# Kernel optimization log

Hardware: AMD Instinct MI355X
Metric: run time of the kernel (lower is better)

## Reference

```python
import jax, jax.numpy as jnp
import numpy as np

HARMONICS = 5


def _harmonic_basis(x):
    k = jnp.arange(1, HARMONICS + 1, dtype=x.dtype)            # [H]
    kx = x[..., None] * k                                       # [B, D, H]
    sc = jnp.stack([jnp.sin(kx), jnp.cos(kx)], axis=-1)         # [B, D, H, 2]
    sc = sc.reshape(*x.shape, 2 * HARMONICS)                    # interleaved sin/cos
    ones = jnp.ones((*x.shape, 1), dtype=x.dtype)
    return jnp.concatenate([ones, sc], axis=-1)                 # [B, D, 2H+1]


def setup_inputs() -> dict:
    key = jax.random.key(0)
    k1, k2, k3 = jax.random.split(key, 3)
    B, D, F, H = 16384, 256, 11, 256
    x = jax.random.normal(k1, (B, D), dtype=jnp.float32)
    W = jax.random.normal(k2, (D, F, H), dtype=jnp.float32) * (1.0 / np.sqrt(F))
    b = jax.random.normal(k3, (D, H), dtype=jnp.float32) * 0.01
    return {"x": x, "W": W, "b": b}


def reference(x, W, b) -> jnp.ndarray:
    # basis expansion per feature, batched small GEMM, summed over features
    basis = _harmonic_basis(x)                                  # [B, D, F]
    out = jnp.einsum('bdf,dfh->bh', basis, W)                   # sum over features fused
    out = out + jnp.sum(b, axis=0)                              # sum of per-feature biases
    return out
```

## Files before the change

kernel.cpp:

```cpp
#include <hip/hip_runtime.h>
#include <hip/hip_bf16.h>


#define BDIM 16384
#define DDIM 256
#define HOUT 256
#define KTOT 2560
#define NKT  80
#define BM 64
#define BN 128

typedef __bf16 bf16x8 __attribute__((ext_vector_type(8)));
typedef float floatx4 __attribute__((ext_vector_type(4)));

__device__ __forceinline__ unsigned short f2bf(float f) {
    unsigned int u = __float_as_uint(f);
    return (unsigned short)((u + 0x7FFFu + ((u >> 16) & 1u)) >> 16);
}

__device__ __forceinline__ unsigned int pkbf(float a, float b) {
    __hip_bfloat162 r = __float22bfloat162_rn(make_float2(a, b));
    return *reinterpret_cast<unsigned int*>(&r);
}

__global__ void prep_kernel(const float* __restrict__ W, const float* __restrict__ bias,
                            unsigned short* __restrict__ Wfrag, float* __restrict__ c_part) {
    const int bid = blockIdx.x;
    const int t = threadIdx.x;
    if (bid < NKT) {
        const int kt = bid;
        const int dtile = kt / 10;
        const int f = kt - dtile * 10 + 1;
        const float* wsrc = W + ((size_t)(dtile * 32) * 11 + f) * 256 + t;
        union { unsigned short s[32]; int4 v[4]; } buf;
#pragma unroll
        for (int dd = 0; dd < 32; ++dd)
            buf.s[dd] = f2bf(wsrc[(size_t)dd * 11 * 256]);
        int4* dst = (int4*)(Wfrag + ((size_t)kt * 256 + t) * 32);
#pragma unroll
        for (int v = 0; v < 4; ++v) dst[v] = buf.v[v];
    } else {
        const int p = bid - NKT;
        float acc = 0.f;
#pragma unroll
        for (int dd = 0; dd < 32; ++dd) {
            const int d = p * 32 + dd;
            acc += W[(size_t)(d * 11) * 256 + t] + bias[(size_t)d * 256 + t];
        }
        c_part[p * 256 + t] = acc;
    }
}

__global__ __launch_bounds__(256, 2)
void kan_gemm(const float* __restrict__ x, const unsigned short* __restrict__ Wfrag,
              const float* __restrict__ c_part, float* __restrict__ out) {
    __shared__ unsigned short As[10 * 4 * 512];

    const int t = threadIdx.x;
    const int m0 = blockIdx.x * BM;
    const int h0 = blockIdx.y * BN;

    const int lane = t & 63;
    const int wave = t >> 6;
    const int wr = wave >> 1;
    const int wc = wave & 1;
    const int l15 = lane & 15;
    const int koff = lane >> 4;

    const int m_a = lane;
    const int q = wave;
    const int it_w = m_a >> 4;
    const int slot = (m_a & 15) + 16 * q;

    floatx4 acc[2][4];
#pragma unroll
    for (int i = 0; i < 2; ++i)
#pragma unroll
        for (int j = 0; j < 4; ++j)
            acc[i][j] = (floatx4){0.f, 0.f, 0.f, 0.f};

    const float* xrow = x + (size_t)(m0 + m_a) * DDIM;
    const unsigned short* bbase = Wfrag + (size_t)(h0 + wc * 64 + l15) * 32 + koff * 8;

    float4 xa = *(const float4*)(xrow + q * 8);
    float4 xb = *(const float4*)(xrow + q * 8 + 4);

    for (int dtile = 0; dtile < 8; ++dtile) {
        float xv[8] = {xa.x, xa.y, xa.z, xa.w, xb.x, xb.y, xb.z, xb.w};
        float sc[8], cc[8], sp[8], cp[8], t2c[8];
#pragma unroll
        for (int j = 0; j < 8; ++j) {
            __sincosf(xv[j], &sc[j], &cc[j]);
            t2c[j] = cc[j] + cc[j];
            sp[j] = 0.f;
            cp[j] = 1.f;
        }
#pragma unroll
        for (int k = 1; k <= 5; ++k) {
            union { unsigned int u[4]; int4 v; } vs, vc;
#pragma unroll
            for (int p = 0; p < 4; ++p) {
                vs.u[p] = pkbf(sc[2 * p], sc[2 * p + 1]);
                vc.u[p] = pkbf(cc[2 * p], cc[2 * p + 1]);
            }
            *(int4*)(&As[((2 * k - 2) * 4 + it_w) * 512 + slot * 8]) = vs.v;
            *(int4*)(&As[((2 * k - 1) * 4 + it_w) * 512 + slot * 8]) = vc.v;
            if (k < 5) {
#pragma unroll
                for (int j = 0; j < 8; ++j) {
                    const float ns = t2c[j] * sc[j] - sp[j];
                    const float nc = t2c[j] * cc[j] - cp[j];
                    sp[j] = sc[j]; cp[j] = cc[j];
                    sc[j] = ns;   cc[j] = nc;
                }
            }
        }
        __syncthreads();

        if (dtile < 7) {
            xa = *(const float4*)(xrow + (dtile + 1) * 32 + q * 8);
            xb = *(const float4*)(xrow + (dtile + 1) * 32 + q * 8 + 4);
        }

        const unsigned short* bkt = bbase + (size_t)(dtile * 10) * 8192;

        bf16x8 bf0[4], bf1[4], af0[2], af1[2];
#pragma unroll
        for (int j = 0; j < 4; ++j)
            bf0[j] = *(const bf16x8*)(bkt + j * 512);
#pragma unroll
        for (int i = 0; i < 2; ++i)
            af0[i] = *(const bf16x8*)(&As[(0 * 4 + wr * 2 + i) * 512 + lane * 8]);

#pragma unroll
        for (int hs = 0; hs < 10; ++hs) {
            bf16x8* bnext = (hs & 1) ? bf0 : bf1;
            bf16x8* anext = (hs & 1) ? af0 : af1;
            if (hs < 9) {
#pragma unroll
                for (int j = 0; j < 4; ++j)
                    bnext[j] = *(const bf16x8*)(bkt + (size_t)(hs + 1) * 8192 + j * 512);
#pragma unroll
                for (int i = 0; i < 2; ++i)
                    anext[i] = *(const bf16x8*)(&As[((hs + 1) * 4 + wr * 2 + i) * 512 + lane * 8]);
            }
            const bf16x8* bcur = (hs & 1) ? bf1 : bf0;
            const bf16x8* acur = (hs & 1) ? af1 : af0;
#pragma unroll
            for (int i = 0; i < 2; ++i)
#pragma unroll
                for (int j = 0; j < 4; ++j)
                    acc[i][j] = __builtin_amdgcn_mfma_f32_16x16x32_bf16(acur[i], bcur[j], acc[i][j], 0, 0, 0);
        }
        __syncthreads();
    }

    float cj[4];
#pragma unroll
    for (int j = 0; j < 4; ++j) {
        const int col = h0 + wc * 64 + j * 16 + l15;
        float s = 0.f;
#pragma unroll
        for (int p = 0; p < 8; ++p) s += c_part[p * 256 + col];
        cj[j] = s;
    }
#pragma unroll
    for (int i = 0; i < 2; ++i) {
        const int row0 = m0 + wr * 32 + i * 16 + koff * 4;
#pragma unroll
        for (int j = 0; j < 4; ++j) {
            const int col = h0 + wc * 64 + j * 16 + l15;
#pragma unroll
            for (int r = 0; r < 4; ++r)
                out[(size_t)(row0 + r) * HOUT + col] = acc[i][j][r] + cj[j];
        }
    }
}

extern "C" void kernel_launch(void* const* d_in, const int* in_sizes, int n_in,
                              void* d_out, int out_size, void* d_ws, size_t ws_size,
                              hipStream_t stream) {
    const float* x = (const float*)d_in[0];
    const float* W = (const float*)d_in[1];
    const float* b = (const float*)d_in[2];
    float* out = (float*)d_out;

    unsigned short* Wfrag = (unsigned short*)d_ws;
    float* c_part = (float*)((char*)d_ws + (size_t)NKT * 256 * 32 * 2);

    prep_kernel<<<NKT + 8, 256, 0, stream>>>(W, b, Wfrag, c_part);
    kan_gemm<<<dim3(BDIM / BM, HOUT / BN), 256, 0, stream>>>(x, Wfrag, c_part, out);
}
```

Measured before the change: 117.0 us.

## Double-buffer basis tiles, split harmonics into halves, enlarge M tile to 128

Raises the block M tile from 64 to 128 rows, so each wave now holds a 4x4 grid of MFMA accumulators, and double-buffers the shared-memory A tile. Each dtile's ten harmonic K-slices are split into two halves of five. The next half's basis values are generated while the current half is multiplied, which removes one barrier-separated generation phase per dtile. The W fragment order is permuted with FMAP so each half matches the harmonics a thread computes directly through closed-form multiple-angle identities. The cost is more accumulator registers, since the occupancy hint of 2 blocks is dropped, plus a different rounding path for the harmonics.

```diff
diff --git a/kernel.cpp b/kernel.cpp
--- a/kernel.cpp
+++ b/kernel.cpp
@@ -2,13 +2,10 @@
 #include <hip/hip_bf16.h>
 
 
-#define BDIM 16384
+#define HOUT 256
 #define DDIM 256
-#define HOUT 256
 #define KTOT 2560
 #define NKT  80
-#define BM 64
-#define BN 128
 
 typedef __bf16 bf16x8 __attribute__((ext_vector_type(8)));
 typedef float floatx4 __attribute__((ext_vector_type(4)));
@@ -22,6 +19,8 @@
     __hip_bfloat162 r = __float22bfloat162_rn(make_float2(a, b));
     return *reinterpret_cast<unsigned int*>(&r);
 }
+
+__device__ __constant__ int FMAP[10] = {1, 2, 5, 6, 9, 3, 4, 7, 8, 10};
 
 __global__ void prep_kernel(const float* __restrict__ W, const float* __restrict__ bias,
                             unsigned short* __restrict__ Wfrag, float* __restrict__ c_part) {
@@ -30,7 +29,7 @@
     if (bid < NKT) {
         const int kt = bid;
         const int dtile = kt / 10;
-        const int f = kt - dtile * 10 + 1;
+        const int f = FMAP[kt - dtile * 10];
         const float* wsrc = W + ((size_t)(dtile * 32) * 11 + f) * 256 + t;
         union { unsigned short s[32]; int4 v[4]; } buf;
 #pragma unroll
@@ -51,14 +50,51 @@
     }
 }
 
-__global__ __launch_bounds__(256, 2)
+__device__ __forceinline__ void harm5(float xv, float v[5], int halfsel) {
+    float s1, c1;
+    __sincosf(xv, &s1, &c1);
+    const float t2 = c1 + c1;
+    const float c2 = __builtin_fmaf(t2, c1, -1.f);
+    const float tc = c2 + c2;
+    if (halfsel == 0) {
+        const float s3 = __builtin_fmaf(tc, s1, s1);
+        const float c3 = __builtin_fmaf(tc, c1, -c1);
+        const float s5 = __builtin_fmaf(tc, s3, -s1);
+        v[0] = s1; v[1] = c1; v[2] = s3; v[3] = c3; v[4] = s5;
+    } else {
+        const float s2 = t2 * s1;
+        const float s4 = tc * s2;
+        const float c4 = __builtin_fmaf(tc, c2, -1.f);
+        const float c5 = __builtin_fmaf(c4, c1, -s4 * s1);
+        v[0] = s2; v[1] = c2; v[2] = s4; v[3] = c4; v[4] = c5;
+    }
+}
+
+__device__ __forceinline__ void gen_octet(unsigned short* dst, const float4 xa,
+                                          const float4 xb, int halfsel) {
+    union { unsigned int u[4]; int4 q; } fr[5];
+    const float xs[8] = {xa.x, xa.y, xa.z, xa.w, xb.x, xb.y, xb.z, xb.w};
+#pragma unroll
+    for (int p = 0; p < 4; ++p) {
+        float va[5], vb[5];
+        harm5(xs[2 * p], va, halfsel);
+        harm5(xs[2 * p + 1], vb, halfsel);
+#pragma unroll
+        for (int hs = 0; hs < 5; ++hs) fr[hs].u[p] = pkbf(va[hs], vb[hs]);
+    }
+#pragma unroll
+    for (int hs = 0; hs < 5; ++hs)
+        *(int4*)(dst + hs * 4096) = fr[hs].q;
+}
+
+__global__ __launch_bounds__(256)
 void kan_gemm(const float* __restrict__ x, const unsigned short* __restrict__ Wfrag,
               const float* __restrict__ c_part, float* __restrict__ out) {
-    __shared__ unsigned short As[10 * 4 * 512];
+    __shared__ unsigned short As[2][5 * 8 * 512];
 
     const int t = threadIdx.x;
-    const int m0 = blockIdx.x * BM;
-    const int h0 = blockIdx.y * BN;
+    const int m0 = blockIdx.x * 128;
+    const int h0 = blockIdx.y * 128;
 
     const int lane = t & 63;
     const int wave = t >> 6;
@@ -67,90 +103,81 @@
     const int l15 = lane & 15;
     const int koff = lane >> 4;
 
-    const int m_a = lane;
-    const int q = wave;
-    const int it_w = m_a >> 4;
-    const int slot = (m_a & 15) + 16 * q;
-
-    floatx4 acc[2][4];
-#pragma unroll
-    for (int i = 0; i < 2; ++i)
+    const int gm = t & 127;
+    const int gob = (t >> 7) * 2;
+    const int goff0 = (gm >> 4) * 512 + ((gm & 15) + 16 * gob) * 8;
+    const int goff1 = (gm >> 4) * 512 + ((gm & 15) + 16 * (gob + 1)) * 8;
+
+    floatx4 acc[4][4];
+#pragma unroll
+    for (int il = 0; il < 4; ++il)
 #pragma unroll
         for (int j = 0; j < 4; ++j)
-            acc[i][j] = (floatx4){0.f, 0.f, 0.f, 0.f};
-
-    const float* xrow = x + (size_t)(m0 + m_a) * DDIM;
+            acc[il][j] = (floatx4){0.f, 0.f, 0.f, 0.f};
+
+    const float* xrow = x + (size_t)(m0 + gm) * DDIM + gob * 8;
     const unsigned short* bbase = Wfrag + (size_t)(h0 + wc * 64 + l15) * 32 + koff * 8;
 
-    float4 xa = *(const float4*)(xrow + q * 8);
-    float4 xb = *(const float4*)(xrow + q * 8 + 4);
-
-    for (int dtile = 0; dtile < 8; ++dtile) {
-        float xv[8] = {xa.x, xa.y, xa.z, xa.w, xb.x, xb.y, xb.z, xb.w};
-        float sc[8], cc[8], sp[8], cp[8], t2c[8];
-#pragma unroll
-        for (int j = 0; j < 8; ++j) {
-            __sincosf(xv[j], &sc[j], &cc[j]);
-            t2c[j] = cc[j] + cc[j];
-            sp[j] = 0.f;
-            cp[j] = 1.f;
-        }
-#pragma unroll
-        for (int k = 1; k <= 5; ++k) {
-            union { unsigned int u[4]; int4 v; } vs, vc;
-#pragma unroll
-            for (int p = 0; p < 4; ++p) {
-                vs.u[p] = pkbf(sc[2 * p], sc[2 * p + 1]);
-                vc.u[p] = pkbf(cc[2 * p], cc[2 * p + 1]);
+    float4 xq0, xq1, xq2, xq3;
+
+    {
+        const float* xp = xrow;
+        xq0 = *(const float4*)(xp);
+        xq1 = *(const float4*)(xp + 4);
+        xq2 = *(const float4*)(xp + 8);
+        xq3 = *(const float4*)(xp + 12);
+        gen_octet(&As[0][goff0], xq0, xq1, 0);
+        gen_octet(&As[0][goff1], xq2, xq3, 0);
+    }
+    __syncthreads();
+
+    for (int h = 0; h < 16; ++h) {
+        unsigned short* bufc = As[h & 1];
+        const unsigned short* bkt = bbase + (size_t)(5 * h) * 8192;
+
+        bf16x8 bc[4], bn[4], ac[4], an[4];
+#pragma unroll
+        for (int j = 0; j < 4; ++j)
+            bc[j] = *(const bf16x8*)(bkt + j * 512);
+#pragma unroll
+        for (int il = 0; il < 4; ++il)
+            ac[il] = *(const bf16x8*)(&bufc[(wr * 4 + il) * 512 + lane * 8]);
+
+        if (h < 15) {
+            const int hn = h + 1;
+            if ((hn & 1) == 0) {
+                const float* xp = xrow + (hn >> 1) * 32;
+                xq0 = *(const float4*)(xp);
+                xq1 = *(const float4*)(xp + 4);
+                xq2 = *(const float4*)(xp + 8);
+                xq3 = *(const float4*)(xp + 12);
             }
-            *(int4*)(&As[((2 * k - 2) * 4 + it_w) * 512 + slot * 8]) = vs.v;
-            *(int4*)(&As[((2 * k - 1) * 4 + it_w) * 512 + slot * 8]) = vc.v;
-            if (k < 5) {
-#pragma unroll
-                for (int j = 0; j < 8; ++j) {
-                    const float ns = t2c[j] * sc[j] - sp[j];
-                    const float nc = t2c[j] * cc[j] - cp[j];
-                    sp[j] = sc[j]; cp[j] = cc[j];
-                    sc[j] = ns;   cc[j] = nc;
-                }
+            unsigned short* bufn = As[hn & 1];
+            gen_octet(&bufn[goff0], xq0, xq1, hn & 1);
+            gen_octet(&bufn[goff1], xq2, xq3, hn & 1);
+        }
+
+#pragma unroll
+        for (int hs = 0; hs < 5; ++hs) {
+            if (hs < 4) {
+#pragma unroll
+                for (int j = 0; j < 4; ++j)
+                    bn[j] = *(const bf16x8*)(bkt + (size_t)(hs + 1) * 8192 + j * 512);
+#pragma unroll
+                for (int il = 0; il < 4; ++il)
+                    an[il] = *(const bf16x8*)(&bufc[((hs + 1) * 8 + wr * 4 + il) * 512 + lane * 8]);
             }
-        }
-        __syncthreads();
-
-        if (dtile < 7) {
-            xa = *(const float4*)(xrow + (dtile + 1) * 32 + q * 8);
-            xb = *(const float4*)(xrow + (dtile + 1) * 32 + q * 8 + 4);
-        }
-
-        const unsigned short* bkt = bbase + (size_t)(dtile * 10) * 8192;
-
-        bf16x8 bf0[4], bf1[4], af0[2], af1[2];
-#pragma unroll
-        for (int j = 0; j < 4; ++j)
-            bf0[j] = *(const bf16x8*)(bkt + j * 512);
-#pragma unroll
-        for (int i = 0; i < 2; ++i)
-            af0[i] = *(const bf16x8*)(&As[(0 * 4 + wr * 2 + i) * 512 + lane * 8]);
-
-#pragma unroll
-        for (int hs = 0; hs < 10; ++hs) {
-            bf16x8* bnext = (hs & 1) ? bf0 : bf1;
-            bf16x8* anext = (hs & 1) ? af0 : af1;
-            if (hs < 9) {
+#pragma unroll
+            for (int il = 0; il < 4; ++il)
 #pragma unroll
                 for (int j = 0; j < 4; ++j)
-                    bnext[j] = *(const bf16x8*)(bkt + (size_t)(hs + 1) * 8192 + j * 512);
-#pragma unroll
-                for (int i = 0; i < 2; ++i)
-                    anext[i] = *(const bf16x8*)(&As[((hs + 1) * 4 + wr * 2 + i) * 512 + lane * 8]);
+                    acc[il][j] = __builtin_amdgcn_mfma_f32_16x16x32_bf16(ac[il], bc[j], acc[il][j], 0, 0, 0);
+            if (hs < 4) {
+#pragma unroll
+                for (int j = 0; j < 4; ++j) bc[j] = bn[j];
+#pragma unroll
+                for (int il = 0; il < 4; ++il) ac[il] = an[il];
             }
-            const bf16x8* bcur = (hs & 1) ? bf1 : bf0;
-            const bf16x8* acur = (hs & 1) ? af1 : af0;
-#pragma unroll
-            for (int i = 0; i < 2; ++i)
-#pragma unroll
-                for (int j = 0; j < 4; ++j)
-                    acc[i][j] = __builtin_amdgcn_mfma_f32_16x16x32_bf16(acur[i], bcur[j], acc[i][j], 0, 0, 0);
         }
         __syncthreads();
     }
@@ -165,14 +192,14 @@
         cj[j] = s;
     }
 #pragma unroll
-    for (int i = 0; i < 2; ++i) {
-        const int row0 = m0 + wr * 32 + i * 16 + koff * 4;
+    for (int il = 0; il < 4; ++il) {
+        const int row0 = m0 + (wr * 4 + il) * 16 + koff * 4;
 #pragma unroll
         for (int j = 0; j < 4; ++j) {
             const int col = h0 + wc * 64 + j * 16 + l15;
 #pragma unroll
             for (int r = 0; r < 4; ++r)
-                out[(size_t)(row0 + r) * HOUT + col] = acc[i][j][r] + cj[j];
+                out[(size_t)(row0 + r) * HOUT + col] = acc[il][j][r] + cj[j];
         }
     }
 }
@@ -189,5 +216,5 @@
     float* c_part = (float*)((char*)d_ws + (size_t)NKT * 256 * 32 * 2);
 
     prep_kernel<<<NKT + 8, 256, 0, stream>>>(W, b, Wfrag, c_part);
-    kan_gemm<<<dim3(BDIM / BM, HOUT / BN), 256, 0, stream>>>(x, Wfrag, c_part, out);
-}
+    kan_gemm<<<dim3(16384 / 128, 2), 256, 0, stream>>>(x, Wfrag, c_part, out);
+}
```

Result: slower. 123.8 us (+5.8%).
